# Optimization experiments

Hardware: AMD Instinct MI355X
Metric: run time of the kernel (lower is better)

The kernel has to match this reference:

```python
import jax, jax.numpy as jnp
import numpy as np

B, T, E, H = 2, 1024, 1024, 16
D = E // H
HEAVY_RATIO = 0.1
RECENT_RATIO = 0.1
QUANT_RATIO = 0.5  # module-level global `quantized_ratio`
NEG = jnp.finfo(jnp.float32).min


def setup_inputs() -> dict:
    key = jax.random.key(0)
    ks = jax.random.split(key, 10)
    s = 0.02
    hidden_states = jax.random.normal(ks[0], (B, T, E), jnp.float32)
    causal = jnp.tril(jnp.ones((T, T), bool))
    attention_mask = jnp.broadcast_to(jnp.where(causal, 0.0, NEG).astype(jnp.float32)[None, None], (B, 1, T, T))
    lin = lambda k: (jax.random.normal(k, (E, E), jnp.float32) * s)
    return {
        'hidden_states': hidden_states,
        'attention_mask': attention_mask,
        'Wq': lin(ks[1]), 'bq': jnp.zeros((E,), jnp.float32),
        'Wk': lin(ks[2]), 'bk': jnp.zeros((E,), jnp.float32),
        'Wv': lin(ks[3]), 'bv': jnp.zeros((E,), jnp.float32),
        'Wo': lin(ks[4]), 'bo': jnp.zeros((E,), jnp.float32),
    }


def _heavy_hitter_mask(aw, hb):
    # aw: [BH, T, T] masked attn logits. Faithful to local_heavy_hitter_mask
    # (use_gumbel=False path, no padding). Returns bool mask_bottom [BH, T, T].
    BH, Tt, _ = aw.shape
    tmp = jax.nn.softmax(aw, axis=-1)               # fp32 softmax
    acc = tmp[:, :hb, :].sum(axis=1)                # [BH, T]
    acc = acc * (jnp.arange(Tt) < hb)               # zero cols >= hb
    col_lt_hb = (jnp.arange(Tt) < hb)
    init_block = jnp.broadcast_to(col_lt_hb[None, None, :], (BH, hb, Tt))
    row_ids = jnp.arange(BH)[:, None]
    cols = jnp.arange(Tt)

    def step(acc, xs):
        row, t = xs                                  # row: [BH, T], t: scalar index
        tmp_i = jax.nn.softmax(row, axis=-1)
        _, idx = jax.lax.top_k(acc, hb - 1)          # heavy-hitter indices [BH, hb-1]
        mb = jnp.zeros((BH, Tt), bool).at[row_ids, idx].set(True)
        mb = mb | (cols == t)[None, :]               # always keep current token
        acc = (acc + tmp_i) * mb                     # accumulate + evict
        return acc, mb

    ts = jnp.arange(hb, Tt)
    rows = jnp.swapaxes(aw[:, hb:, :], 0, 1)         # [T-hb, BH, T]
    _, mbs = jax.lax.scan(step, acc, (rows, ts))
    mask = jnp.concatenate([init_block, jnp.swapaxes(mbs, 0, 1)], axis=1)
    return jnp.tril(mask)


def reference(hidden_states, attention_mask, Wq, bq, Wk, bk, Wv, bv, Wo, bo):
    scaling = D ** -0.5
    shape = lambda x: jnp.transpose(x.reshape(B, T, H, D), (0, 2, 1, 3)).reshape(B * H, T, D)
    q = shape((hidden_states @ Wq + bq) * scaling)
    k = shape(hidden_states @ Wk + bk)
    v = shape(hidden_states @ Wv + bv)

    aw = jnp.einsum('btd,bsd->bts', q, k)                      # [BH, T, T]
    aw = aw.reshape(B, H, T, T) + attention_mask               # additive causal mask
    aw = jnp.maximum(aw, NEG).reshape(B * H, T, T)

    hb = int(HEAVY_RATIO * T)
    qt = int(hb * QUANT_RATIO)
    hb = hb + qt                                               # inflated heavy budget
    recent = int(RECENT_RATIO * T)

    mask_bottom = _heavy_hitter_mask(jax.lax.stop_gradient(aw), hb)
    recent_mask = jnp.triu(jnp.ones((T, T), bool), -recent)    # recent window
    mask = jnp.tril(mask_bottom | recent_mask[None])

    # torch code recomputes the identical masked logits; reuse aw
    aw = jnp.where(mask, aw, jnp.min(attention_mask))
    probs = jax.nn.softmax(aw, axis=-1)
    out = jnp.einsum('bts,bsd->btd', probs, v)                 # [BH, T, D]
    out = jnp.transpose(out.reshape(B, H, T, D), (0, 2, 1, 3)).reshape(B, T, E)
    return out @ Wo + bo
```

## Files before the change

kernel.cpp:

```cpp
#include <hip/hip_runtime.h>
#include <hip/hip_bf16.h>
#include <stdint.h>

#define TT 1024
#define EE 1024
#define HH 16
#define DD 64
#define BHN 32
#define HB 153
#define RECW 102
#define RING 8
#define INFLT 4
#define NEGF (-3.4028234663852886e38f)

typedef unsigned long long ull;
typedef __attribute__((ext_vector_type(8))) short bf16x8;
typedef __attribute__((ext_vector_type(4))) float f32x4;

#define OFF_Q  ((size_t)0)
#define OFF_K  (OFF_Q + (size_t)BHN*TT*DD)
#define OFF_V  (OFF_K + (size_t)BHN*TT*DD)
#define OFF_AW (OFF_V + (size_t)BHN*TT*DD)
#define OFF_M  (OFF_AW + (size_t)BHN*TT*TT)
#define OFF_S  (OFF_M + (size_t)BHN*TT)
#define OFF_AO (OFF_S + (size_t)BHN*TT)
#define OFF_END (OFF_AO + (size_t)BHN*TT*DD)

__device__ __forceinline__ ushort f2bf(float x) {
  unsigned u = __float_as_uint(x);
  u = (u + 0x7FFF + ((u >> 16) & 1)) >> 16;
  return (ushort)u;
}
__device__ __forceinline__ float bf2f(ushort h) {
  return __uint_as_float((unsigned)h << 16);
}

__global__ __launch_bounds__(256) void k_pmm(const float* __restrict__ X,
    const float* __restrict__ W, const float* __restrict__ bias,
    float* __restrict__ Y, float scale, int mode) {
  __shared__ ushort Ah[64][72], Al[64][72];
  __shared__ ushort Bh[64][72], Bl[64][72];
  int tid = threadIdx.x, lane = tid & 63, wid = tid >> 6;
  int r = tid >> 2, c0 = (tid & 3) * 16;
  int r0 = blockIdx.y * 64, n0 = blockIdx.x * 64;

  f32x4 acc[4];
  #pragma unroll
  for (int nc = 0; nc < 4; ++nc) acc[nc] = (f32x4){0.f, 0.f, 0.f, 0.f};

  for (int k0 = 0; k0 < EE; k0 += 64) {
    __syncthreads();
    {
      const float4* xs = (const float4*)(X + (size_t)(r0 + r) * EE + k0 + c0);
      #pragma unroll
      for (int q4 = 0; q4 < 4; ++q4) {
        float4 v = xs[q4];
        float f[4] = {v.x, v.y, v.z, v.w};
        ushort hi[4], lo[4];
        #pragma unroll
        for (int u = 0; u < 4; ++u) {
          hi[u] = f2bf(f[u]);
          lo[u] = f2bf(f[u] - bf2f(hi[u]));
        }
        *(unsigned*)&Ah[r][c0 + q4*4]     = (unsigned)hi[0] | ((unsigned)hi[1] << 16);
        *(unsigned*)&Ah[r][c0 + q4*4 + 2] = (unsigned)hi[2] | ((unsigned)hi[3] << 16);
        *(unsigned*)&Al[r][c0 + q4*4]     = (unsigned)lo[0] | ((unsigned)lo[1] << 16);
        *(unsigned*)&Al[r][c0 + q4*4 + 2] = (unsigned)lo[2] | ((unsigned)lo[3] << 16);
      }
    }
    {
      const float4* wsrc = (const float4*)(W + (size_t)(k0 + r) * EE + n0 + c0);
      #pragma unroll
      for (int q4 = 0; q4 < 4; ++q4) {
        float4 v = wsrc[q4];
        float f[4] = {v.x, v.y, v.z, v.w};
        #pragma unroll
        for (int u = 0; u < 4; ++u) {
          ushort hi = f2bf(f[u]);
          ushort lo = f2bf(f[u] - bf2f(hi));
          int c = c0 + q4*4 + u;
          Bh[c][r] = hi;
          Bl[c][r] = lo;
        }
      }
    }
    __syncthreads();
    #pragma unroll
    for (int kb = 0; kb < 2; ++kb) {
      bf16x8 ah = *(const bf16x8*)&Ah[wid*16 + (lane & 15)][kb*32 + (lane >> 4)*8];
      bf16x8 al = *(const bf16x8*)&Al[wid*16 + (lane & 15)][kb*32 + (lane >> 4)*8];
      #pragma unroll
      for (int nc = 0; nc < 4; ++nc) {
        bf16x8 bh_ = *(const bf16x8*)&Bh[nc*16 + (lane & 15)][kb*32 + (lane >> 4)*8];
        bf16x8 bl_ = *(const bf16x8*)&Bl[nc*16 + (lane & 15)][kb*32 + (lane >> 4)*8];
        acc[nc] = __builtin_amdgcn_mfma_f32_16x16x32_bf16(ah, bh_, acc[nc], 0, 0, 0);
        acc[nc] = __builtin_amdgcn_mfma_f32_16x16x32_bf16(al, bh_, acc[nc], 0, 0, 0);
        acc[nc] = __builtin_amdgcn_mfma_f32_16x16x32_bf16(ah, bl_, acc[nc], 0, 0, 0);
      }
    }
  }

  int rowbase = wid*16 + (lane >> 4)*4;
  #pragma unroll
  for (int nc = 0; nc < 4; ++nc) {
    int c = n0 + nc*16 + (lane & 15);
    float bv = bias[c];
    #pragma unroll
    for (int qq = 0; qq < 4; ++qq) {
      int rr = r0 + rowbase + qq;
      float val = (acc[nc][qq] + bv) * scale;
      int b_ = rr >> 10, t_ = rr & 1023, h_ = c >> 6, d_ = c & 63;
      if (mode == 1) {
        Y[(((size_t)(b_*HH + h_) * TT) + t_) * DD + d_] = val;
      } else if (mode == 2) {
        ((ushort*)Y)[(((size_t)(b_*HH + h_) * TT) + t_) * DD + d_] = f2bf(val);
      } else {
        Y[(size_t)rr * EE + c] = val;
      }
    }
  }
}

__global__ __launch_bounds__(256) void k_qk_mfma(const float* __restrict__ q,
    const float* __restrict__ k, float* __restrict__ aw) {
  int bh = blockIdx.y, tt = blockIdx.x;
  int t0 = tt * 64;
  int tid = threadIdx.x, lane = tid & 63, wid = tid >> 6;
  int r = tid >> 2, c0 = (tid & 3) * 16;
  __shared__ ushort Qh[64][72], Ql[64][72];
  __shared__ ushort Kh[64][72], Kl[64][72];
  const float* qb = q + (size_t)bh * TT * DD;
  const float* kb = k + (size_t)bh * TT * DD;
  float* awb = aw + (size_t)bh * TT * TT;

  {
    const float4* xs = (const float4*)(qb + (size_t)(t0 + r) * DD + c0);
    #pragma unroll
    for (int q4 = 0; q4 < 4; ++q4) {
      float4 v = xs[q4];
      float f[4] = {v.x, v.y, v.z, v.w};
      ushort hi[4], lo[4];
      #pragma unroll
      for (int u = 0; u < 4; ++u) {
        hi[u] = f2bf(f[u]);
        lo[u] = f2bf(f[u] - bf2f(hi[u]));
      }
      *(unsigned*)&Qh[r][c0 + q4*4]     = (unsigned)hi[0] | ((unsigned)hi[1] << 16);
      *(unsigned*)&Qh[r][c0 + q4*4 + 2] = (unsigned)hi[2] | ((unsigned)hi[3] << 16);
      *(unsigned*)&Ql[r][c0 + q4*4]     = (unsigned)lo[0] | ((unsigned)lo[1] << 16);
      *(unsigned*)&Ql[r][c0 + q4*4 + 2] = (unsigned)lo[2] | ((unsigned)lo[3] << 16);
    }
  }

  for (int st = 0; st <= tt; ++st) {
    __syncthreads();
    {
      const float4* xs = (const float4*)(kb + (size_t)(st * 64 + r) * DD + c0);
      #pragma unroll
      for (int q4 = 0; q4 < 4; ++q4) {
        float4 v = xs[q4];
        float f[4] = {v.x, v.y, v.z, v.w};
        ushort hi[4], lo[4];
        #pragma unroll
        for (int u = 0; u < 4; ++u) {
          hi[u] = f2bf(f[u]);
          lo[u] = f2bf(f[u] - bf2f(hi[u]));
        }
        *(unsigned*)&Kh[r][c0 + q4*4]     = (unsigned)hi[0] | ((unsigned)hi[1] << 16);
        *(unsigned*)&Kh[r][c0 + q4*4 + 2] = (unsigned)hi[2] | ((unsigned)hi[3] << 16);
        *(unsigned*)&Kl[r][c0 + q4*4]     = (unsigned)lo[0] | ((unsigned)lo[1] << 16);
        *(unsigned*)&Kl[r][c0 + q4*4 + 2] = (unsigned)lo[2] | ((unsigned)lo[3] << 16);
      }
    }
    __syncthreads();
    f32x4 acc[4];
    #pragma unroll
    for (int nc = 0; nc < 4; ++nc) acc[nc] = (f32x4){0.f, 0.f, 0.f, 0.f};
    #pragma unroll
    for (int kb2 = 0; kb2 < 2; ++kb2) {
      bf16x8 ah = *(const bf16x8*)&Qh[wid*16 + (lane & 15)][kb2*32 + (lane >> 4)*8];
      bf16x8 al = *(const bf16x8*)&Ql[wid*16 + (lane & 15)][kb2*32 + (lane >> 4)*8];
      #pragma unroll
      for (int nc = 0; nc < 4; ++nc) {
        bf16x8 bh_ = *(const bf16x8*)&Kh[nc*16 + (lane & 15)][kb2*32 + (lane >> 4)*8];
        bf16x8 bl_ = *(const bf16x8*)&Kl[nc*16 + (lane & 15)][kb2*32 + (lane >> 4)*8];
        acc[nc] = __builtin_amdgcn_mfma_f32_16x16x32_bf16(ah, bh_, acc[nc], 0, 0, 0);
        acc[nc] = __builtin_amdgcn_mfma_f32_16x16x32_bf16(al, bh_, acc[nc], 0, 0, 0);
        acc[nc] = __builtin_amdgcn_mfma_f32_16x16x32_bf16(ah, bl_, acc[nc], 0, 0, 0);
      }
    }
    int rowbase = wid*16 + (lane >> 4)*4;
    #pragma unroll
    for (int nc = 0; nc < 4; ++nc) {
      int s = st * 64 + nc*16 + (lane & 15);
      #pragma unroll
      for (int qq = 0; qq < 4; ++qq) {
        int t_ = t0 + rowbase + qq;
        awb[(size_t)t_ * TT + s] = acc[nc][qq];
      }
    }
  }
}

__global__ __launch_bounds__(256) void k_softmax(float* __restrict__ aw) {
  int bh = blockIdx.y;
  int wid = threadIdx.x >> 6, lane = threadIdx.x & 63;
  int t = blockIdx.x * 4 + wid;
  float* row = aw + ((size_t)bh * TT + t) * TT;
  float vals[16];
  float m = NEGF;
  #pragma unroll
  for (int i = 0; i < 16; ++i) {
    int j = lane + 64*i;
    vals[i] = (j <= t) ? row[j] : NEGF;
    m = fmaxf(m, vals[i]);
  }
  for (int o = 32; o; o >>= 1) m = fmaxf(m, __shfl_xor(m, o));
  float s = 0.f;
  #pragma unroll
  for (int i = 0; i < 16; ++i) {
    int j = lane + 64*i;
    if (j <= t) { vals[i] = expf(vals[i] - m); s += vals[i]; }
  }
  for (int o = 32; o; o >>= 1) s += __shfl_xor(s, o);
  float inv = 1.0f / s;
  #pragma unroll
  for (int i = 0; i < 16; ++i) {
    int j = lane + 64*i;
    if (j <= t) row[j] = vals[i] * inv;
  }
}

__global__ __launch_bounds__(256) void k_init_acc(const float* __restrict__ p,
    float* __restrict__ initacc) {
  int bh = blockIdx.x;
  int c = threadIdx.x;
  float val = 0.f;
  if (c < HB) {
    const float* pb = p + (size_t)bh * TT * TT;
    for (int i = c; i < HB; ++i)
      val += pb[(size_t)i * TT + c];
  }
  initacc[(size_t)bh * 256 + c] = val;
}

#define DPP_HOP(ctrl)                                                        \
  {                                                                          \
    unsigned tt = (unsigned)__builtin_amdgcn_update_dpp(                     \
        (int)0xFFFFFFFFu, (int)x, (ctrl), 0xF, 0xF, false);                  \
    x = x < tt ? x : tt;                                                     \
  }
__device__ __forceinline__ unsigned wave_min_u32(unsigned x) {
  DPP_HOP(0x111)
  DPP_HOP(0x112)
  DPP_HOP(0x114)
  DPP_HOP(0x118)
  DPP_HOP(0x142)
  DPP_HOP(0x143)
  return (unsigned)__builtin_amdgcn_readlane((int)x, 63);
}

__device__ __forceinline__ void gload_lds16(const float* gsrc, float* ldst) {
  __builtin_amdgcn_global_load_lds(
      (const __attribute__((address_space(1))) unsigned int*)gsrc,
      (__attribute__((address_space(3))) unsigned int*)ldst,
      16, 0, 0);
}

__global__ __launch_bounds__(128) void k_scan(const float* __restrict__ p,
    const float* __restrict__ initacc, int* __restrict__ evict_g) {
  int bh = blockIdx.x;
  int tid = threadIdx.x;
  int lane = tid & 63;
  const float* pb = p + (size_t)bh * TT * TT;
  __shared__ float ring[RING][TT];
  __shared__ int ev[TT];
  __shared__ volatile int rdyf[RING];
  __shared__ volatile int donef;
  for (int i = tid; i < TT; i += 128) ev[i] = 0x7fffffff;
  if (tid < RING) rdyf[tid] = -1;
  if (tid == 0) donef = -1;
  __syncthreads();

  if (tid >= 64) {
    #pragma unroll
    for (int r = 0; r < INFLT; ++r) {
      const float* srcrow = pb + (size_t)(HB + r) * TT;
      float* slotbase = ring[(HB + r) & (RING - 1)];
      #pragma unroll
      for (int j = 0; j < 4; ++j)
        gload_lds16(srcrow + j * 256 + lane * 4, slotbase + j * 256);
    }
    for (int r = HB; r < TT; ++r) {
      asm volatile("s_waitcnt vmcnt(12)" ::: "memory");
      if (lane == 0) rdyf[r & (RING - 1)] = r;
      int rn = r + INFLT;
      if (rn - RING >= HB) {
        while (donef < rn - RING) { }
      }
      int rsrc = rn < TT ? rn : TT - 1;
      const float* srcrow = pb + (size_t)rsrc * TT;
      float* slotbase = ring[rn & (RING - 1)];
      #pragma unroll
      for (int j = 0; j < 4; ++j)
        gload_lds16(srcrow + j * 256 + lane * 4, slotbase + j * 256);
    }
  } else {
    bool act2 = lane < (HB - 128);
    int col[3]; float sc[3];
    col[0] = lane;
    col[1] = 64 + lane;
    col[2] = act2 ? (128 + lane) : 0;
    sc[0] = initacc[(size_t)bh * 256 + lane];
    sc[1] = initacc[(size_t)bh * 256 + 64 + lane];
    sc[2] = act2 ? initacc[(size_t)bh * 256 + 128 + lane] : 0.f;
    int fpeek = -2;
    for (int t = HB; t < TT; ++t) {
      int slot = t & (RING - 1);
      if (fpeek != t) {
        while (rdyf[slot] != t) { }
      }
      asm volatile("" ::: "memory");
      const float* rb = ring[slot];
      float r0 = rb[col[0]];
      float r1 = rb[col[1]];
      float r2 = rb[col[2]];
      float rd = rb[t];
      fpeek = rdyf[(t + 1) & (RING - 1)];
      unsigned b0 = __float_as_uint(sc[0]);
      unsigned b1 = __float_as_uint(sc[1]);
      unsigned b2 = act2 ? __float_as_uint(sc[2]) : 0xFFFFFFFFu;
      unsigned mn = b0 < b1 ? b0 : b1; mn = mn < b2 ? mn : b2;
      unsigned mstar = wave_min_u32(mn);
      unsigned c0k = (b0 == mstar) ? (unsigned)(1023 - col[0]) : 0xFFFFFFFFu;
      unsigned c1k = (b1 == mstar) ? (unsigned)(1023 - col[1]) : 0xFFFFFFFFu;
      unsigned c2k = (act2 && b2 == mstar) ? (unsigned)(1023 - col[2]) : 0xFFFFFFFFu;
      unsigned cm = c0k < c1k ? c0k : c1k; cm = cm < c2k ? cm : c2k;
      int cstar = 1023 - (int)wave_min_u32(cm);
      if (b0 == mstar && col[0] == cstar) { ev[col[0]] = t; col[0] = t; sc[0] = rd; }
      else sc[0] += r0;
      if (b1 == mstar && col[1] == cstar) { ev[col[1]] = t; col[1] = t; sc[1] = rd; }
      else sc[1] += r1;
      if (act2) {
        if (b2 == mstar && col[2] == cstar) { ev[col[2]] = t; col[2] = t; sc[2] = rd; }
        else sc[2] += r2;
      }
      asm volatile("" ::: "memory");
      if (lane == 0) donef = t;
    }
  }

  __syncthreads();
  int4* dst4 = (int4*)(evict_g + (size_t)bh * TT);
  const int4* src4 = (const int4*)ev;
  for (int i = tid; i < TT/4; i += 128) dst4[i] = src4[i];
}

__global__ __launch_bounds__(256) void k_pv(const float* __restrict__ p,
    const int* __restrict__ evict_g, const ushort* __restrict__ vbf,
    float* __restrict__ ao) {
  int bh = blockIdx.y, tt = blockIdx.x;
  int tid = threadIdx.x, lane = tid & 63, wid = tid >> 6;
  int t0 = tt * 64;
  __shared__ ushort PA[64][72];
  __shared__ ushort VT[64][72];
  __shared__ float rowsum[64];
  __shared__ int et[TT];
  ((int4*)et)[tid] = ((const int4*)(evict_g + (size_t)bh * TT))[tid];
  if (tid < 64) rowsum[tid] = 0.f;
  const float* pb = p + ((size_t)bh * TT + t0) * TT;
  const ushort* vb = vbf + (size_t)bh * TT * DD;

  f32x4 acc[4];
  #pragma unroll
  for (int nc = 0; nc < 4; ++nc) acc[nc] = (f32x4){0.f, 0.f, 0.f, 0.f};

  int r = tid >> 2;
  int c0 = (tid & 3) * 16;
  int tg = t0 + r;
  __syncthreads();

  for (int st = 0; st <= tt; ++st) {
    const float* prow = pb + (size_t)r * TT + st * 64 + c0;
    float part = 0.f;
    ushort tmp16[16];
    #pragma unroll
    for (int q4 = 0; q4 < 4; ++q4) {
      float4 pv4 = *(const float4*)(prow + q4 * 4);
      float vals[4] = {pv4.x, pv4.y, pv4.z, pv4.w};
      #pragma unroll
      for (int u = 0; u < 4; ++u) {
        int j = st * 64 + c0 + q4 * 4 + u;
        bool allow = (j <= tg) && ((et[j] > tg) || (j + RECW >= tg));
        float mv = allow ? vals[u] : 0.f;
        part += mv;
        tmp16[q4 * 4 + u] = f2bf(mv);
      }
    }
    #pragma unroll
    for (int w2 = 0; w2 < 8; ++w2) {
      unsigned pk = (unsigned)tmp16[w2 * 2] | ((unsigned)tmp16[w2 * 2 + 1] << 16);
      *(unsigned*)&PA[r][c0 + w2 * 2] = pk;
    }
    part += __shfl_xor(part, 1);
    part += __shfl_xor(part, 2);
    if ((tid & 3) == 0) rowsum[r] += part;
    {
      const unsigned* vrow32 = (const unsigned*)(vb + (size_t)(st * 64 + r) * DD + c0);
      #pragma unroll
      for (int u = 0; u < 8; ++u) {
        unsigned vv = vrow32[u];
        VT[c0 + u * 2][r] = (ushort)(vv & 0xFFFF);
        VT[c0 + u * 2 + 1][r] = (ushort)(vv >> 16);
      }
    }
    __syncthreads();
    #pragma unroll
    for (int kb = 0; kb < 2; ++kb) {
      bf16x8 af = *(const bf16x8*)&PA[wid * 16 + (lane & 15)][kb * 32 + (lane >> 4) * 8];
      #pragma unroll
      for (int nc = 0; nc < 4; ++nc) {
        bf16x8 bfr = *(const bf16x8*)&VT[nc * 16 + (lane & 15)][kb * 32 + (lane >> 4) * 8];
        acc[nc] = __builtin_amdgcn_mfma_f32_16x16x32_bf16(af, bfr, acc[nc], 0, 0, 0);
      }
    }
    __syncthreads();
  }

  int b_ = bh >> 4, h_ = bh & 15;
  int rl = wid * 16 + (lane >> 4) * 4;
  #pragma unroll
  for (int nc = 0; nc < 4; ++nc) {
    int d = nc * 16 + (lane & 15);
    #pragma unroll
    for (int qq = 0; qq < 4; ++qq) {
      int rr = rl + qq;
      float outv = acc[nc][qq] / rowsum[rr];
      ao[((size_t)b_ * TT + (t0 + rr)) * EE + h_ * DD + d] = outv;
    }
  }
}

extern "C" void kernel_launch(void* const* d_in, const int* in_sizes, int n_in,
                              void* d_out, int out_size, void* d_ws, size_t ws_size,
                              hipStream_t stream) {
  const float* hs = (const float*)d_in[0];
  const float* Wq = (const float*)d_in[2];
  const float* bq = (const float*)d_in[3];
  const float* Wk = (const float*)d_in[4];
  const float* bk = (const float*)d_in[5];
  const float* Wv = (const float*)d_in[6];
  const float* bv = (const float*)d_in[7];
  const float* Wo = (const float*)d_in[8];
  const float* bo = (const float*)d_in[9];
  float* out = (float*)d_out;

  float* ws = (float*)d_ws;
  float* q  = ws + OFF_Q;
  float* k  = ws + OFF_K;
  float* v  = ws + OFF_V;
  float* aw = ws + OFF_AW;
  float* ao = ws + OFF_AO;
  float* initacc = ws + OFF_END;
  int* evict = (int*)(ws + OFF_END + (size_t)BHN * 256);

  dim3 gproj(16, 32);
  k_pmm<<<gproj, 256, 0, stream>>>(hs, Wq, bq, q, 0.125f, 1);
  k_pmm<<<gproj, 256, 0, stream>>>(hs, Wk, bk, k, 1.0f, 1);
  k_pmm<<<gproj, 256, 0, stream>>>(hs, Wv, bv, v, 1.0f, 2);

  dim3 gqk(16, BHN);
  k_qk_mfma<<<gqk, 256, 0, stream>>>(q, k, aw);

  dim3 grs(TT/4, BHN);
  k_softmax<<<grs, 256, 0, stream>>>(aw);

  k_init_acc<<<BHN, 256, 0, stream>>>(aw, initacc);

  k_scan<<<BHN, 128, 0, stream>>>(aw, initacc, evict);

  dim3 gpv(16, BHN);
  k_pv<<<gpv, 256, 0, stream>>>(aw, evict, (const ushort*)v, ao);

  k_pmm<<<gproj, 256, 0, stream>>>(ao, Wo, bo, out, 1.0f, 0);
}
```

Measured before the change: 660.8 us.

## Deepen scan ring prefetch and software-pipeline eviction selection

Doubles the LDS ring buffer and the number of in-flight row loads in the sequential heavy-hitter scan, so global-to-LDS latency is hidden better. It also restructures the consumer loop so the argmin selection (wave reductions) for step t+1 runs right after step t's update, with the row reads issued early. The equality test is simplified to a column comparison only. The larger ring uses more LDS, and the rewritten loop must keep exact tie-breaking semantics.

```diff
diff --git a/kernel.cpp b/kernel.cpp
--- a/kernel.cpp
+++ b/kernel.cpp
@@ -9,8 +9,8 @@
 #define BHN 32
 #define HB 153
 #define RECW 102
-#define RING 8
-#define INFLT 4
+#define RING 16
+#define INFLT 8
 #define NEGF (-3.4028234663852886e38f)
 
 typedef unsigned long long ull;
@@ -292,7 +292,7 @@
         gload_lds16(srcrow + j * 256 + lane * 4, slotbase + j * 256);
     }
     for (int r = HB; r < TT; ++r) {
-      asm volatile("s_waitcnt vmcnt(12)" ::: "memory");
+      asm volatile("s_waitcnt vmcnt(28)" ::: "memory");
       if (lane == 0) rdyf[r & (RING - 1)] = r;
       int rn = r + INFLT;
       if (rn - RING >= HB) {
@@ -307,46 +307,60 @@
     }
   } else {
     bool act2 = lane < (HB - 128);
-    int col[3]; float sc[3];
-    col[0] = lane;
-    col[1] = 64 + lane;
-    col[2] = act2 ? (128 + lane) : 0;
-    sc[0] = initacc[(size_t)bh * 256 + lane];
-    sc[1] = initacc[(size_t)bh * 256 + 64 + lane];
-    sc[2] = act2 ? initacc[(size_t)bh * 256 + 128 + lane] : 0.f;
-    int fpeek = -2;
-    for (int t = HB; t < TT; ++t) {
-      int slot = t & (RING - 1);
-      if (fpeek != t) {
-        while (rdyf[slot] != t) { }
-      }
-      asm volatile("" ::: "memory");
-      const float* rb = ring[slot];
-      float r0 = rb[col[0]];
-      float r1 = rb[col[1]];
-      float r2 = rb[col[2]];
-      float rd = rb[t];
-      fpeek = rdyf[(t + 1) & (RING - 1)];
-      unsigned b0 = __float_as_uint(sc[0]);
-      unsigned b1 = __float_as_uint(sc[1]);
-      unsigned b2 = act2 ? __float_as_uint(sc[2]) : 0xFFFFFFFFu;
+    int col0 = lane, col1 = 64 + lane, col2 = act2 ? (128 + lane) : 0;
+    float sc0 = initacc[(size_t)bh * 256 + lane];
+    float sc1 = initacc[(size_t)bh * 256 + 64 + lane];
+    float sc2 = act2 ? initacc[(size_t)bh * 256 + 128 + lane] : 0.f;
+
+    while (rdyf[HB & (RING - 1)] != HB) { }
+    asm volatile("" ::: "memory");
+    int fpeek = rdyf[(HB + 1) & (RING - 1)];
+    float r0, r1, r2, rd;
+    {
+      const float* rb = ring[HB & (RING - 1)];
+      r0 = rb[col0]; r1 = rb[col1]; r2 = rb[col2]; rd = rb[HB];
+    }
+    int cstar;
+    {
+      unsigned b0 = __float_as_uint(sc0);
+      unsigned b1 = __float_as_uint(sc1);
+      unsigned b2 = act2 ? __float_as_uint(sc2) : 0xFFFFFFFFu;
       unsigned mn = b0 < b1 ? b0 : b1; mn = mn < b2 ? mn : b2;
       unsigned mstar = wave_min_u32(mn);
-      unsigned c0k = (b0 == mstar) ? (unsigned)(1023 - col[0]) : 0xFFFFFFFFu;
-      unsigned c1k = (b1 == mstar) ? (unsigned)(1023 - col[1]) : 0xFFFFFFFFu;
-      unsigned c2k = (act2 && b2 == mstar) ? (unsigned)(1023 - col[2]) : 0xFFFFFFFFu;
+      unsigned c0k = (b0 == mstar) ? (unsigned)(1023 - col0) : 0xFFFFFFFFu;
+      unsigned c1k = (b1 == mstar) ? (unsigned)(1023 - col1) : 0xFFFFFFFFu;
+      unsigned c2k = (act2 && b2 == mstar) ? (unsigned)(1023 - col2) : 0xFFFFFFFFu;
       unsigned cm = c0k < c1k ? c0k : c1k; cm = cm < c2k ? cm : c2k;
-      int cstar = 1023 - (int)wave_min_u32(cm);
-      if (b0 == mstar && col[0] == cstar) { ev[col[0]] = t; col[0] = t; sc[0] = rd; }
-      else sc[0] += r0;
-      if (b1 == mstar && col[1] == cstar) { ev[col[1]] = t; col[1] = t; sc[1] = rd; }
-      else sc[1] += r1;
+      cstar = 1023 - (int)wave_min_u32(cm);
+    }
+
+    for (int t = HB; t < TT; ++t) {
+      if (col0 == cstar) { ev[col0] = t; col0 = t; sc0 = rd; } else sc0 += r0;
+      if (col1 == cstar) { ev[col1] = t; col1 = t; sc1 = rd; } else sc1 += r1;
       if (act2) {
-        if (b2 == mstar && col[2] == cstar) { ev[col[2]] = t; col[2] = t; sc[2] = rd; }
-        else sc[2] += r2;
-      }
-      asm volatile("" ::: "memory");
+        if (col2 == cstar) { ev[col2] = t; col2 = t; sc2 = rd; } else sc2 += r2;
+      }
       if (lane == 0) donef = t;
+      if (t + 1 < TT) {
+        int slot = (t + 1) & (RING - 1);
+        if (fpeek != t + 1) {
+          while (rdyf[slot] != t + 1) { }
+        }
+        asm volatile("" ::: "memory");
+        fpeek = rdyf[(t + 2) & (RING - 1)];
+        const float* rb = ring[slot];
+        r0 = rb[col0]; r1 = rb[col1]; r2 = rb[col2]; rd = rb[t + 1];
+        unsigned b0 = __float_as_uint(sc0);
+        unsigned b1 = __float_as_uint(sc1);
+        unsigned b2 = act2 ? __float_as_uint(sc2) : 0xFFFFFFFFu;
+        unsigned mn = b0 < b1 ? b0 : b1; mn = mn < b2 ? mn : b2;
+        unsigned mstar = wave_min_u32(mn);
+        unsigned c0k = (b0 == mstar) ? (unsigned)(1023 - col0) : 0xFFFFFFFFu;
+        unsigned c1k = (b1 == mstar) ? (unsigned)(1023 - col1) : 0xFFFFFFFFu;
+        unsigned c2k = (act2 && b2 == mstar) ? (unsigned)(1023 - col2) : 0xFFFFFFFFu;
+        unsigned cm = c0k < c1k ? c0k : c1k; cm = cm < c2k ? cm : c2k;
+        cstar = 1023 - (int)wave_min_u32(cm);
+      }
     }
   }
 
@@ -482,5 +496,6 @@
   dim3 gpv(16, BHN);
   k_pv<<<gpv, 256, 0, stream>>>(aw, evict, (const ushort*)v, ao);
 
-  k_pmm<<<gproj, 256, 0, stream>>>(ao, Wo, bo, out, 1.0f, 0);
-}
+  dim3 gout(16, 32);
+  k_pmm<<<gout, 256, 0, stream>>>(ao, Wo, bo, out, 1.0f, 0);
+}
```

Measured after the change: 632.1 us. 1.05x faster.
